# Performance work log

Hardware: AMD Instinct MI355X
Metric: run time of the kernel (lower is better)

## Reference

```python
import jax, jax.numpy as jnp
import numpy as np

DX = 1.0
DY = 1.0
W_DIV = 1e9
W_SMOOTH = 10.0
W_STD = 100.0
EPS = 1e-10


def _corner(a, i, j, k):
    # slice dims 2,3,4: 0 -> [0:-1], 1 -> [1:]
    sl = lambda b: slice(1, None) if b else slice(0, -1)
    return a[:, :, sl(i), sl(j), sl(k)]


def setup_inputs() -> dict:
    key = jax.random.key(0)
    k1, k2 = jax.random.split(key)
    outputs = jax.random.normal(k1, (2, 1, 256, 256, 64), dtype=jnp.float32)
    targets = jax.random.normal(k2, (2, 3, 256, 256, 64), dtype=jnp.float32)
    return {"outputs": outputs, "targets": targets}


def _loss(outputs, targets):
    bx, by, bz = targets[:, 0:1], targets[:, 1:2], targets[:, 2:3]
    z = outputs[:, 0:1]

    # vertical thickness and smoothness of its square
    dz = z[..., 1:] - z[..., :-1]
    dz2 = dz ** 2
    lap = (6 * dz2[:, :, 1:-1, 1:-1, 1:-1]
           - dz2[:, :, :-2, 1:-1, 1:-1] - dz2[:, :, 2:, 1:-1, 1:-1]
           - dz2[:, :, 1:-1, :-2, 1:-1] - dz2[:, :, 1:-1, 2:, 1:-1]
           - dz2[:, :, 1:-1, 1:-1, 2:] - dz2[:, :, 1:-1, 1:-1, :-2])
    loss_smooth = jnp.mean(lap ** 2)

    # per-(batch, channel, z) std over the spatial plane (unbiased, matching torch.std)
    loss_std = jnp.mean(jnp.std(dz, axis=(2, 3), ddof=1))

    # 8 cell corners for each field
    corners = lambda a: {(i, j, k): _corner(a, i, j, k)
                         for i in (0, 1) for j in (0, 1) for k in (0, 1)}
    BX, BY, BZ, Z = corners(bx), corners(by), corners(bz), corners(z)

    az = lambda a, b: jnp.abs(Z[a] - Z[b])
    num = (0.25 * (BX[1,0,0] + BX[1,1,0] + BX[1,0,1] + BX[1,1,1]) * DY * 0.5 * (az((1,0,1),(1,0,0)) + az((1,1,1),(1,1,0)))
           - 0.25 * (BX[0,0,0] + BX[0,1,0] + BX[0,0,1] + BX[0,1,1]) * DY * 0.5 * (az((0,0,1),(0,0,0)) + az((0,1,1),(0,1,0)))
           + 0.25 * (BY[0,1,0] + BY[1,1,0] + BY[0,1,1] + BY[1,1,1]) * DX * 0.5 * (az((0,1,1),(0,1,0)) + az((1,1,1),(1,1,0)))
           - 0.25 * (BY[0,0,0] + BY[1,0,0] + BY[0,0,1] + BY[1,0,1]) * DX * 0.5 * (az((0,0,1),(0,0,0)) + az((1,0,1),(1,0,0)))
           + 0.25 * (BZ[0,0,1] + BZ[0,1,1] + BZ[1,0,1] + BZ[1,1,1]) * DX * DY
           - 0.25 * (BZ[0,0,0] + BZ[0,1,0] + BZ[1,0,0] + BZ[1,1,0]) * DX * DY
           + (BX[0,0,1] + BX[1,0,1] + BX[1,1,1]) * DY * (Z[0,0,1] - Z[1,0,1]) / 6
           + (BX[0,1,1] + BX[1,1,1] + BX[1,0,1]) * DY * (Z[0,1,1] - Z[1,1,1]) / 6
           + (BY[1,0,1] + BY[1,1,1] + BY[0,1,1]) * DX * (Z[1,0,1] - Z[1,1,1]) / 6
           + (BY[0,0,1] + BY[0,1,1] + BY[1,1,1]) * DX * (Z[0,0,1] - Z[0,1,1]) / 6
           - (BX[0,0,0] + BX[1,0,0] + BX[1,1,0]) * DY * (Z[0,0,0] - Z[1,0,0]) / 6
           - (BX[0,1,0] + BX[1,1,0] + BX[1,0,0]) * DY * (Z[0,1,0] - Z[1,1,0]) / 6
           - (BY[1,0,0] + BY[1,1,0] + BY[0,1,0]) * DX * (Z[1,0,0] - Z[1,1,0]) / 6
           - (BY[0,0,0] + BY[0,1,0] + BY[1,1,0]) * DX * (Z[0,0,0] - Z[0,1,0]) / 6)

    sum8 = lambda C: sum(C.values())
    den = ((sum8(BX) * 0.125) ** 2 + (sum8(BY) * 0.125) ** 2
           + (sum8(BZ) * 0.125) ** 2 + EPS)
    loss_div = jnp.mean(num ** 2 / den)

    return loss_div * W_DIV, loss_smooth * W_SMOOTH + loss_std * W_STD


def reference(outputs, targets):
    return _loss(outputs, targets)
```

## Files before the change

### kernel.cpp

```cpp
#include <hip/hip_runtime.h>
#include <math.h>


__global__ __launch_bounds__(512) void zero_ws_kernel(float* ws) {
    for (int i = threadIdx.x; i < 32 * 258; i += 512) ws[i] = 0.0f;
}

__global__ __launch_bounds__(256, 4) void fused_loss_kernel(
    const float* __restrict__ zin, const float* __restrict__ tg,
    float* __restrict__ ws)
{
    __shared__ float r1[4][64];
    __shared__ float r2[4][64];
    __shared__ float rsc[4][2];

    const int tid  = threadIdx.x;
    const int lane = tid & 63;
    const int w    = tid >> 6;

    const int bb   = blockIdx.x >> 14;
    const int rest = blockIdx.x & 16383;
    const int tx   = rest & 127;
    const int ty   = rest >> 7;
    const int x    = (tx << 1) | (w >> 1);
    const int y    = (ty << 1) | (w & 1);

    const float* zb = zin + ((size_t)bb << 22);
    const int xp = x < 255 ? x + 1 : 255;
    const int yp = y < 255 ? y + 1 : 255;

    float zC  = zb[x  * 16384 + y  * 64 + lane];
    float zE  = zb[xp * 16384 + y  * 64 + lane];
    float zN  = zb[x  * 16384 + yp * 64 + lane];
    float zNE = zb[xp * 16384 + yp * 64 + lane];

    float zCp  = __shfl_down(zC,  1, 64);
    float zEp  = __shfl_down(zE,  1, 64);
    float zNp  = __shfl_down(zN,  1, 64);
    float zNEp = __shfl_down(zNE, 1, 64);

    float dz   = zCp  - zC;
    float dzE  = zEp  - zE;
    float dzN  = zNp  - zN;
    float dzNE = zNEp - zNE;

    float s1 = (lane < 63) ? dz : 0.0f;
    float s2 = (lane < 63) ? dz * dz : 0.0f;

    float sm = 0.0f;
    if (x >= 1 && x <= 254 && y >= 1 && y <= 254) {
        float zW  = zb[(x - 1) * 16384 + y * 64 + lane];
        float zS  = zb[x * 16384 + (y - 1) * 64 + lane];
        float zWp = __shfl_down(zW, 1, 64);
        float zSp = __shfl_down(zS, 1, 64);
        float dzW = zWp - zW;
        float dzS = zSp - zS;
        float dzm = __shfl_up(dz, 1, 64);
        float dzp = __shfl_down(dz, 1, 64);
        if (lane >= 1 && lane <= 61) {
            float lap = 6.0f * dz * dz
                      - dzW * dzW - dzE * dzE
                      - dzS * dzS - dzN * dzN
                      - dzm * dzm - dzp * dzp;
            sm = lap * lap;
        }
    }

    float dv = 0.0f;
    if (x < 255 && y < 255) {
        const float* bB = tg + (((size_t)bb * 3) << 22) + x * 16384 + y * 64 + lane;
        float bx00 = bB[0];
        float bx10 = bB[16384];
        float bx01 = bB[64];
        float bx11 = bB[16448];
        const float* bY = bB + 4194304;
        float by00 = bY[0];
        float by10 = bY[16384];
        float by01 = bY[64];
        float by11 = bY[16448];
        const float* bZ = bB + 8388608;
        float bz00 = bZ[0];
        float bz10 = bZ[16384];
        float bz01 = bZ[64];
        float bz11 = bZ[16448];

        float bx00p = __shfl_down(bx00, 1, 64);
        float bx10p = __shfl_down(bx10, 1, 64);
        float bx01p = __shfl_down(bx01, 1, 64);
        float bx11p = __shfl_down(bx11, 1, 64);
        float by00p = __shfl_down(by00, 1, 64);
        float by10p = __shfl_down(by10, 1, 64);
        float by01p = __shfl_down(by01, 1, 64);
        float by11p = __shfl_down(by11, 1, 64);
        float bz00p = __shfl_down(bz00, 1, 64);
        float bz10p = __shfl_down(bz10, 1, 64);
        float bz01p = __shfl_down(bz01, 1, 64);
        float bz11p = __shfl_down(bz11, 1, 64);

        if (lane < 63) {
            float adz00 = fabsf(dz),  adz10 = fabsf(dzE);
            float adz01 = fabsf(dzN), adz11 = fabsf(dzNE);

            float num =
                0.125f * ( (bx10 + bx10p + bx11 + bx11p) * (adz10 + adz11)
                         - (bx00 + bx00p + bx01 + bx01p) * (adz00 + adz01)
                         + (by01 + by01p + by11 + by11p) * (adz01 + adz11)
                         - (by00 + by00p + by10 + by10p) * (adz00 + adz10) )
              + 0.25f * ( (bz00p + bz10p + bz01p + bz11p)
                        - (bz00  + bz10  + bz01  + bz11) );

            const float c6 = 1.0f / 6.0f;
            num += c6 * ( (bx00p + bx10p + bx11p) * (zCp - zEp)
                        + (bx01p + bx11p + bx10p) * (zNp - zNEp)
                        + (by10p + by11p + by01p) * (zEp - zNEp)
                        + (by00p + by01p + by11p) * (zCp - zNp)
                        - (bx00 + bx10 + bx11) * (zC - zE)
                        - (bx01 + bx11 + bx10) * (zN - zNE)
                        - (by10 + by11 + by01) * (zE - zNE)
                        - (by00 + by01 + by11) * (zC - zN) );

            float sbx = bx00 + bx00p + bx10 + bx10p
                      + bx01 + bx01p + bx11 + bx11p;
            float sby = by00 + by00p + by10 + by10p
                      + by01 + by01p + by11 + by11p;
            float sbz = bz00 + bz00p + bz10 + bz10p
                      + bz01 + bz01p + bz11 + bz11p;
            float den = 0.015625f * (sbx * sbx + sby * sby + sbz * sbz) + 1e-10f;
            dv = num * num / den;
        }
    }

    #pragma unroll
    for (int off = 32; off > 0; off >>= 1) {
        sm += __shfl_down(sm, off, 64);
        dv += __shfl_down(dv, off, 64);
    }
    r1[w][lane] = s1;
    r2[w][lane] = s2;
    if (lane == 0) { rsc[w][0] = sm; rsc[w][1] = dv; }
    __syncthreads();

    if (tid < 64) {
        float a   = r1[0][tid] + r1[1][tid] + r1[2][tid] + r1[3][tid];
        float b2r = r2[0][tid] + r2[1][tid] + r2[2][tid] + r2[3][tid];
        float* sl = ws + (blockIdx.x & 31) * 258;
        if (tid < 63) {
            atomicAdd(&sl[2 + bb * 64 + tid],   a);
            atomicAdd(&sl[130 + bb * 64 + tid], b2r);
        }
        if (tid == 0) atomicAdd(&sl[0], rsc[0][0] + rsc[1][0] + rsc[2][0] + rsc[3][0]);
        if (tid == 1) atomicAdd(&sl[1], rsc[0][1] + rsc[1][1] + rsc[2][1] + rsc[3][1]);
    }
}

__global__ __launch_bounds__(128) void finalize_kernel(const float* __restrict__ ws,
                                                       float* __restrict__ out)
{
    __shared__ double red[128];
    const int t = threadIdx.x;
    double stdv = 0.0;
    {
        int k = t & 63, bb = t >> 6;
        if (k < 63) {
            double s1 = 0.0, s2 = 0.0;
            for (int p = 0; p < 32; ++p) {
                s1 += (double)ws[p * 258 + 2 + bb * 64 + k];
                s2 += (double)ws[p * 258 + 130 + bb * 64 + k];
            }
            const double N = 65536.0;
            double var = (s2 - s1 * s1 / N) / (N - 1.0);
            stdv = sqrt(var > 0.0 ? var : 0.0);
        }
    }
    red[t] = stdv;
    __syncthreads();
    for (int off = 64; off > 0; off >>= 1) {
        if (t < off) red[t] += red[t + off];
        __syncthreads();
    }
    if (t == 0) {
        double smt = 0.0, dvt = 0.0;
        for (int p = 0; p < 32; ++p) {
            smt += (double)ws[p * 258 + 0];
            dvt += (double)ws[p * 258 + 1];
        }
        double loss_std    = red[0] / 126.0;
        double loss_smooth = smt / (2.0 * 254.0 * 254.0 * 61.0);
        double loss_div    = dvt / (2.0 * 255.0 * 255.0 * 63.0);
        out[0] = (float)(loss_div * 1e9);
        out[1] = (float)(loss_smooth * 10.0 + loss_std * 100.0);
    }
}

extern "C" void kernel_launch(void* const* d_in, const int* in_sizes, int n_in,
                              void* d_out, int out_size, void* d_ws, size_t ws_size,
                              hipStream_t stream) {
    const float* z  = (const float*)d_in[0];
    const float* tg = (const float*)d_in[1];
    float* out = (float*)d_out;
    float* ws  = (float*)d_ws;

    zero_ws_kernel<<<1, 512, 0, stream>>>(ws);
    fused_loss_kernel<<<32768, 256, 0, stream>>>(z, tg, ws);
    finalize_kernel<<<1, 128, 0, stream>>>(ws, out);
}
```

Baseline: 202.2 us.

## Process two y-rows per wave to reuse z and field loads across cells

Each wave now handles two consecutive y rows at one x (a block covers 4 x by 2 y) instead of one cell, so the z rows and B-field rows shared by adjacent cells are loaded once and reused in registers. This cuts redundant global and L2 loads per output cell and halves the block count, which also halves the number of per-block atomic reductions. In exchange it raises register pressure and per-thread work, which may lower occupancy under the existing launch bounds.

Measured after the change: 205.8 us. No clear change (+1.8%).

```diff
diff --git a/kernel.cpp b/kernel.cpp
--- a/kernel.cpp
+++ b/kernel.cpp
@@ -18,115 +18,170 @@
     const int lane = tid & 63;
     const int w    = tid >> 6;
 
-    const int bb   = blockIdx.x >> 14;
-    const int rest = blockIdx.x & 16383;
-    const int tx   = rest & 127;
-    const int ty   = rest >> 7;
-    const int x    = (tx << 1) | (w >> 1);
-    const int y    = (ty << 1) | (w & 1);
+    const int bb   = blockIdx.x >> 13;
+    const int rest = blockIdx.x & 8191;
+    const int X    = rest & 63;
+    const int Y    = rest >> 6;
+    const int x    = (X << 2) | w;
+    const int y0   = Y << 1;
 
     const float* zb = zin + ((size_t)bb << 22);
-    const int xp = x < 255 ? x + 1 : 255;
-    const int yp = y < 255 ? y + 1 : 255;
-
-    float zC  = zb[x  * 16384 + y  * 64 + lane];
-    float zE  = zb[xp * 16384 + y  * 64 + lane];
-    float zN  = zb[x  * 16384 + yp * 64 + lane];
-    float zNE = zb[xp * 16384 + yp * 64 + lane];
-
-    float zCp  = __shfl_down(zC,  1, 64);
-    float zEp  = __shfl_down(zE,  1, 64);
-    float zNp  = __shfl_down(zN,  1, 64);
-    float zNEp = __shfl_down(zNE, 1, 64);
-
-    float dz   = zCp  - zC;
-    float dzE  = zEp  - zE;
-    float dzN  = zNp  - zN;
-    float dzNE = zNEp - zNE;
-
-    float s1 = (lane < 63) ? dz : 0.0f;
-    float s2 = (lane < 63) ? dz * dz : 0.0f;
+    const int xp  = x < 255 ? x + 1 : 255;
+    const int y2c = y0 < 254 ? y0 + 2 : 255;
+
+    const float* zr  = zb + x  * 16384 + y0 * 64 + lane;
+    const float* zrE = zb + xp * 16384 + y0 * 64 + lane;
+    float z0  = zr[0];
+    float z1  = zr[64];
+    float z2  = zb[x  * 16384 + y2c * 64 + lane];
+    float zE0 = zrE[0];
+    float zE1 = zrE[64];
+    float zE2 = zb[xp * 16384 + y2c * 64 + lane];
+
+    float z0p  = __shfl_down(z0,  1, 64);
+    float z1p  = __shfl_down(z1,  1, 64);
+    float z2p  = __shfl_down(z2,  1, 64);
+    float zE0p = __shfl_down(zE0, 1, 64);
+    float zE1p = __shfl_down(zE1, 1, 64);
+    float zE2p = __shfl_down(zE2, 1, 64);
+
+    float dz0  = z0p  - z0;
+    float dz1  = z1p  - z1;
+    float dz2  = z2p  - z2;
+    float dzE0 = zE0p - zE0;
+    float dzE1 = zE1p - zE1;
+    float dzE2 = zE2p - zE2;
+
+    float s1 = (lane < 63) ? (dz0 + dz1) : 0.0f;
+    float s2 = (lane < 63) ? (dz0 * dz0 + dz1 * dz1) : 0.0f;
 
     float sm = 0.0f;
-    if (x >= 1 && x <= 254 && y >= 1 && y <= 254) {
-        float zW  = zb[(x - 1) * 16384 + y * 64 + lane];
-        float zS  = zb[x * 16384 + (y - 1) * 64 + lane];
-        float zWp = __shfl_down(zW, 1, 64);
-        float zSp = __shfl_down(zS, 1, 64);
-        float dzW = zWp - zW;
-        float dzS = zSp - zS;
-        float dzm = __shfl_up(dz, 1, 64);
-        float dzp = __shfl_down(dz, 1, 64);
-        if (lane >= 1 && lane <= 61) {
-            float lap = 6.0f * dz * dz
-                      - dzW * dzW - dzE * dzE
-                      - dzS * dzS - dzN * dzN
-                      - dzm * dzm - dzp * dzp;
-            sm = lap * lap;
+    if (x >= 1 && x <= 254) {
+        if (y0 >= 1) {
+            float zW0  = zb[(x - 1) * 16384 + y0 * 64 + lane];
+            float zS   = zb[x * 16384 + (y0 - 1) * 64 + lane];
+            float zW0p = __shfl_down(zW0, 1, 64);
+            float zSp  = __shfl_down(zS,  1, 64);
+            float dzW0 = zW0p - zW0;
+            float dzS  = zSp  - zS;
+            float dzm  = __shfl_up(dz0, 1, 64);
+            float dzp  = __shfl_down(dz0, 1, 64);
+            if (lane >= 1 && lane <= 61) {
+                float lap = 6.0f * dz0 * dz0
+                          - dzW0 * dzW0 - dzE0 * dzE0
+                          - dzS * dzS   - dz1 * dz1
+                          - dzm * dzm   - dzp * dzp;
+                sm += lap * lap;
+            }
+        }
+        if (y0 <= 253) {
+            float zW1  = zb[(x - 1) * 16384 + (y0 + 1) * 64 + lane];
+            float zW1p = __shfl_down(zW1, 1, 64);
+            float dzW1 = zW1p - zW1;
+            float dzm2 = __shfl_up(dz1, 1, 64);
+            float dzp2 = __shfl_down(dz1, 1, 64);
+            if (lane >= 1 && lane <= 61) {
+                float lap = 6.0f * dz1 * dz1
+                          - dzW1 * dzW1 - dzE1 * dzE1
+                          - dz0 * dz0   - dz2 * dz2
+                          - dzm2 * dzm2 - dzp2 * dzp2;
+                sm += lap * lap;
+            }
         }
     }
 
     float dv = 0.0f;
-    if (x < 255 && y < 255) {
-        const float* bB = tg + (((size_t)bb * 3) << 22) + x * 16384 + y * 64 + lane;
-        float bx00 = bB[0];
-        float bx10 = bB[16384];
-        float bx01 = bB[64];
-        float bx11 = bB[16448];
+    if (x < 255) {
+        const float* bB = tg + (((size_t)bb * 3) << 22) + x * 16384 + y0 * 64 + lane;
         const float* bY = bB + 4194304;
-        float by00 = bY[0];
-        float by10 = bY[16384];
-        float by01 = bY[64];
-        float by11 = bY[16448];
         const float* bZ = bB + 8388608;
-        float bz00 = bZ[0];
-        float bz10 = bZ[16384];
-        float bz01 = bZ[64];
-        float bz11 = bZ[16448];
-
-        float bx00p = __shfl_down(bx00, 1, 64);
-        float bx10p = __shfl_down(bx10, 1, 64);
-        float bx01p = __shfl_down(bx01, 1, 64);
-        float bx11p = __shfl_down(bx11, 1, 64);
-        float by00p = __shfl_down(by00, 1, 64);
-        float by10p = __shfl_down(by10, 1, 64);
-        float by01p = __shfl_down(by01, 1, 64);
-        float by11p = __shfl_down(by11, 1, 64);
-        float bz00p = __shfl_down(bz00, 1, 64);
-        float bz10p = __shfl_down(bz10, 1, 64);
-        float bz01p = __shfl_down(bz01, 1, 64);
-        float bz11p = __shfl_down(bz11, 1, 64);
-
+        float bx0  = bB[0],   bxE0 = bB[16384];
+        float bx1  = bB[64],  bxE1 = bB[16448];
+        float by0  = bY[0],   byE0 = bY[16384];
+        float by1  = bY[64],  byE1 = bY[16448];
+        float bz0  = bZ[0],   bzE0 = bZ[16384];
+        float bz1  = bZ[64],  bzE1 = bZ[16448];
+
+        float bx0p  = __shfl_down(bx0,  1, 64);
+        float bxE0p = __shfl_down(bxE0, 1, 64);
+        float bx1p  = __shfl_down(bx1,  1, 64);
+        float bxE1p = __shfl_down(bxE1, 1, 64);
+        float by0p  = __shfl_down(by0,  1, 64);
+        float byE0p = __shfl_down(byE0, 1, 64);
+        float by1p  = __shfl_down(by1,  1, 64);
+        float byE1p = __shfl_down(byE1, 1, 64);
+        float bz0p  = __shfl_down(bz0,  1, 64);
+        float bzE0p = __shfl_down(bzE0, 1, 64);
+        float bz1p  = __shfl_down(bz1,  1, 64);
+        float bzE1p = __shfl_down(bzE1, 1, 64);
+
+        const float c6 = 1.0f / 6.0f;
         if (lane < 63) {
-            float adz00 = fabsf(dz),  adz10 = fabsf(dzE);
-            float adz01 = fabsf(dzN), adz11 = fabsf(dzNE);
+            float adz00 = fabsf(dz0),  adz10 = fabsf(dzE0);
+            float adz01 = fabsf(dz1),  adz11 = fabsf(dzE1);
 
             float num =
-                0.125f * ( (bx10 + bx10p + bx11 + bx11p) * (adz10 + adz11)
-                         - (bx00 + bx00p + bx01 + bx01p) * (adz00 + adz01)
-                         + (by01 + by01p + by11 + by11p) * (adz01 + adz11)
-                         - (by00 + by00p + by10 + by10p) * (adz00 + adz10) )
-              + 0.25f * ( (bz00p + bz10p + bz01p + bz11p)
-                        - (bz00  + bz10  + bz01  + bz11) );
-
-            const float c6 = 1.0f / 6.0f;
-            num += c6 * ( (bx00p + bx10p + bx11p) * (zCp - zEp)
-                        + (bx01p + bx11p + bx10p) * (zNp - zNEp)
-                        + (by10p + by11p + by01p) * (zEp - zNEp)
-                        + (by00p + by01p + by11p) * (zCp - zNp)
-                        - (bx00 + bx10 + bx11) * (zC - zE)
-                        - (bx01 + bx11 + bx10) * (zN - zNE)
-                        - (by10 + by11 + by01) * (zE - zNE)
-                        - (by00 + by01 + by11) * (zC - zN) );
-
-            float sbx = bx00 + bx00p + bx10 + bx10p
-                      + bx01 + bx01p + bx11 + bx11p;
-            float sby = by00 + by00p + by10 + by10p
-                      + by01 + by01p + by11 + by11p;
-            float sbz = bz00 + bz00p + bz10 + bz10p
-                      + bz01 + bz01p + bz11 + bz11p;
+                0.125f * ( (bxE0 + bxE0p + bxE1 + bxE1p) * (adz10 + adz11)
+                         - (bx0  + bx0p  + bx1  + bx1p ) * (adz00 + adz01)
+                         + (by1  + by1p  + byE1 + byE1p) * (adz01 + adz11)
+                         - (by0  + by0p  + byE0 + byE0p) * (adz00 + adz10) )
+              + 0.25f * ( (bz0p + bzE0p + bz1p + bzE1p)
+                        - (bz0  + bzE0  + bz1  + bzE1) );
+
+            num += c6 * ( (bx0p  + bxE0p + bxE1p) * (z0p  - zE0p)
+                        + (bx1p  + bxE1p + bxE0p) * (z1p  - zE1p)
+                        + (byE0p + byE1p + by1p ) * (zE0p - zE1p)
+                        + (by0p  + by1p  + byE1p) * (z0p  - z1p)
+                        - (bx0  + bxE0 + bxE1) * (z0  - zE0)
+                        - (bx1  + bxE1 + bxE0) * (z1  - zE1)
+                        - (byE0 + byE1 + by1 ) * (zE0 - zE1)
+                        - (by0  + by1  + byE1) * (z0  - z1) );
+
+            float sbx = bx0 + bx0p + bxE0 + bxE0p + bx1 + bx1p + bxE1 + bxE1p;
+            float sby = by0 + by0p + byE0 + byE0p + by1 + by1p + byE1 + byE1p;
+            float sbz = bz0 + bz0p + bzE0 + bzE0p + bz1 + bz1p + bzE1 + bzE1p;
             float den = 0.015625f * (sbx * sbx + sby * sby + sbz * sbz) + 1e-10f;
             dv = num * num / den;
+        }
+
+        if (y0 + 1 < 255) {
+            float bx2 = bB[128], bxE2 = bB[16512];
+            float by2 = bY[128], byE2 = bY[16512];
+            float bz2 = bZ[128], bzE2 = bZ[16512];
+            float bx2p  = __shfl_down(bx2,  1, 64);
+            float bxE2p = __shfl_down(bxE2, 1, 64);
+            float by2p  = __shfl_down(by2,  1, 64);
+            float byE2p = __shfl_down(byE2, 1, 64);
+            float bz2p  = __shfl_down(bz2,  1, 64);
+            float bzE2p = __shfl_down(bzE2, 1, 64);
+
+            if (lane < 63) {
+                float adz00 = fabsf(dz1),  adz10 = fabsf(dzE1);
+                float adz01 = fabsf(dz2),  adz11 = fabsf(dzE2);
+
+                float num =
+                    0.125f * ( (bxE1 + bxE1p + bxE2 + bxE2p) * (adz10 + adz11)
+                             - (bx1  + bx1p  + bx2  + bx2p ) * (adz00 + adz01)
+                             + (by2  + by2p  + byE2 + byE2p) * (adz01 + adz11)
+                             - (by1  + by1p  + byE1 + byE1p) * (adz00 + adz10) )
+                  + 0.25f * ( (bz1p + bzE1p + bz2p + bzE2p)
+                            - (bz1  + bzE1  + bz2  + bzE2) );
+
+                num += c6 * ( (bx1p  + bxE1p + bxE2p) * (z1p  - zE1p)
+                            + (bx2p  + bxE2p + bxE1p) * (z2p  - zE2p)
+                            + (byE1p + byE2p + by2p ) * (zE1p - zE2p)
+                            + (by1p  + by2p  + byE2p) * (z1p  - z2p)
+                            - (bx1  + bxE1 + bxE2) * (z1  - zE1)
+                            - (bx2  + bxE2 + bxE1) * (z2  - zE2)
+                            - (byE1 + byE2 + by2 ) * (zE1 - zE2)
+                            - (by1  + by2  + byE2) * (z1  - z2) );
+
+                float sbx = bx1 + bx1p + bxE1 + bxE1p + bx2 + bx2p + bxE2 + bxE2p;
+                float sby = by1 + by1p + byE1 + byE1p + by2 + by2p + byE2 + byE2p;
+                float sbz = bz1 + bz1p + bzE1 + bzE1p + bz2 + bz2p + bzE2 + bzE2p;
+                float den = 0.015625f * (sbx * sbx + sby * sby + sbz * sbz) + 1e-10f;
+                dv += num * num / den;
+            }
         }
     }
 
@@ -201,6 +256,6 @@
     float* ws  = (float*)d_ws;
 
     zero_ws_kernel<<<1, 512, 0, stream>>>(ws);
-    fused_loss_kernel<<<32768, 256, 0, stream>>>(z, tg, ws);
+    fused_loss_kernel<<<16384, 256, 0, stream>>>(z, tg, ws);
     finalize_kernel<<<1, 128, 0, stream>>>(ws, out);
 }
```
